# Kernel tuning notes

Measured on AMD Instinct MI355X. Metric: run time of the kernel, lower is better.

The kernel has to match this reference:

```python
import jax, jax.numpy as jnp
import numpy as np

SPARSITY = 0.5  # cur_sparsity set during training; 0.0 default would make masking a no-op
WEIGHT_BETA = 1.0
MASK_ALPHA1 = 1.0
MASK_ALPHA2 = 1.0


def binarize(mask_scores, sparsity):
    # SparseBinarizer.forward: prune (set to 0) the `num_prune` smallest scores globally.
    num_prune = int(mask_scores.size * sparsity)  # static: sparsity is a Python float
    flat = mask_scores.reshape(-1)
    prune_idx = jnp.argsort(flat)[:num_prune]
    mask = jnp.ones_like(flat).at[prune_idx].set(0.0)
    return mask.reshape(mask_scores.shape)


def setup_inputs() -> dict:
    key = jax.random.key(0)
    ks = jax.random.split(key, 9)
    out_f, in_f, r = 4096, 4096, 8
    tokens = 8192  # batch 4 * seq 2048
    return {
        "x": jax.random.normal(ks[0], (tokens, in_f), dtype=jnp.float32),
        "weight": jax.random.normal(ks[1], (out_f, in_f), dtype=jnp.float32) * 0.02,
        "bias": jax.random.normal(ks[2], (out_f,), dtype=jnp.float32) * 0.02,
        "weight_U": jax.random.normal(ks[3], (out_f, r), dtype=jnp.float32),
        "weight_V": jnp.zeros((r, in_f), dtype=jnp.float32),
        "mask_scores_A": jax.random.normal(ks[4], (out_f, r), dtype=jnp.float32),
        "mask_scores_B": jnp.zeros((r, in_f), dtype=jnp.float32),
        "mask_scores_R": jnp.zeros((out_f,), dtype=jnp.float32),
        "mask_scores_C": jnp.zeros((in_f,), dtype=jnp.float32),
    }


def reference(x, weight, bias, weight_U, weight_V, mask_scores_A, mask_scores_B,
              mask_scores_R, mask_scores_C):
    # weight = W + beta * U @ V   (low-rank weight reconstruction)
    w = weight + WEIGHT_BETA * (weight_U @ weight_V)
    # mask_scores = |w| + a1 * A @ B + a2 * (R[:,None] + C[None,:])
    mask_scores = (jnp.abs(w)
                   + MASK_ALPHA1 * (mask_scores_A @ mask_scores_B)
                   + MASK_ALPHA2 * (mask_scores_R[:, None] + mask_scores_C[None, :]))
    mask = binarize(mask_scores, SPARSITY)
    masked_weight = mask * w  # [out_f, in_f]
    # nn.Linear: x @ W^T + b
    return x @ masked_weight.T + bias
```

## Files before the change

### kernel.cpp

```cpp
#include <hip/hip_runtime.h>
#include <stdint.h>

#define TOKENS 8192
#define OUT_F  4096
#define IN_F   4096
#define RNK    8
#define KPRUNE 8388608u
#define CAP3   16384u

typedef unsigned short u16;
typedef float  f32x4  __attribute__((ext_vector_type(4)));
typedef short  bf16x8 __attribute__((ext_vector_type(8)));
typedef unsigned short u16x4 __attribute__((ext_vector_type(4)));
typedef unsigned short u16x8 __attribute__((ext_vector_type(8)));

#define XB_OFF    0ull
#define WB_OFF    67108864ull
#define CTL_OFF   100663296ull
#define H1_OFF    0
#define H2_OFF    16384
#define CNT3_OFF  32768
#define LIST3_OFF 32772
#define CTL_ZERO_U32 8193

__device__ __forceinline__ u16 f2bf(float f) {
    uint32_t u = __float_as_uint(f);
    u += 0x7fffu + ((u >> 16) & 1u);
    return (u16)(u >> 16);
}

__device__ __forceinline__ uint32_t fkey(float s) {
    uint32_t u = __float_as_uint(s);
    return (u & 0x80000000u) ? ~u : (u | 0x80000000u);
}

__device__ __forceinline__ void hsel(const uint32_t* __restrict__ hist, uint32_t k,
                                     volatile uint32_t* scr,
                                     uint32_t& bin, uint32_t& below)
{
    const int t = threadIdx.x;
    const int lane = t & 63, w = t >> 6;
    uint32_t v[16]; uint32_t s = 0;
#pragma unroll
    for (int j = 0; j < 16; ++j) { v[j] = hist[t*16 + j]; s += v[j]; }
    uint32_t sc = s;
#pragma unroll
    for (int d = 1; d < 64; d <<= 1) {
        uint32_t o = __shfl_up(sc, d, 64);
        if (lane >= d) sc += o;
    }
    if (lane == 63) scr[w] = sc;
    __syncthreads();
    uint32_t woff = 0;
    for (int ww = 0; ww < w; ++ww) woff += scr[ww];
    const uint32_t pre = woff + sc - s;
    if (pre < k && pre + s >= k) {
        uint32_t bb = pre;
#pragma unroll
        for (int j = 0; j < 16; ++j) {
            if (bb < k && bb + v[j] >= k) { scr[4] = (uint32_t)(t*16 + j); scr[5] = bb; }
            bb += v[j];
        }
    }
    __syncthreads();
    bin = scr[4]; below = scr[5];
    __syncthreads();
}

struct S2 { float4 w0, w1; uint4 k0, k1; };
__device__ __forceinline__ S2 score2(const float* __restrict__ W,
                                     const float* __restrict__ V,
                                     const float* __restrict__ B,
                                     const float* __restrict__ C,
                                     const float* uu0, const float* uu1,
                                     const float* aa0, const float* aa1,
                                     float ro0, float ro1, int o0, int i)
{
    const float4 cc = *(const float4*)&C[i];
    float4 w0 = *(const float4*)&W[(size_t)o0*IN_F + i];
    float4 w1 = *(const float4*)&W[(size_t)(o0+1)*IN_F + i];
#pragma unroll
    for (int r = 0; r < RNK; ++r) {
        const float4 v4 = *(const float4*)&V[r*IN_F + i];
        const float a0 = uu0[r], a1 = uu1[r];
        w0.x = fmaf(a0, v4.x, w0.x); w0.y = fmaf(a0, v4.y, w0.y);
        w0.z = fmaf(a0, v4.z, w0.z); w0.w = fmaf(a0, v4.w, w0.w);
        w1.x = fmaf(a1, v4.x, w1.x); w1.y = fmaf(a1, v4.y, w1.y);
        w1.z = fmaf(a1, v4.z, w1.z); w1.w = fmaf(a1, v4.w, w1.w);
    }
    float4 s0, s1;
    s0.x = fabsf(w0.x); s0.y = fabsf(w0.y); s0.z = fabsf(w0.z); s0.w = fabsf(w0.w);
    s1.x = fabsf(w1.x); s1.y = fabsf(w1.y); s1.z = fabsf(w1.z); s1.w = fabsf(w1.w);
#pragma unroll
    for (int r = 0; r < RNK; ++r) {
        const float4 b4 = *(const float4*)&B[r*IN_F + i];
        const float a0 = aa0[r], a1 = aa1[r];
        s0.x = fmaf(a0, b4.x, s0.x); s0.y = fmaf(a0, b4.y, s0.y);
        s0.z = fmaf(a0, b4.z, s0.z); s0.w = fmaf(a0, b4.w, s0.w);
        s1.x = fmaf(a1, b4.x, s1.x); s1.y = fmaf(a1, b4.y, s1.y);
        s1.z = fmaf(a1, b4.z, s1.z); s1.w = fmaf(a1, b4.w, s1.w);
    }
    s0.x += ro0 + cc.x; s0.y += ro0 + cc.y; s0.z += ro0 + cc.z; s0.w += ro0 + cc.w;
    s1.x += ro1 + cc.x; s1.y += ro1 + cc.y; s1.z += ro1 + cc.z; s1.w += ro1 + cc.w;
    S2 o;
    o.w0 = w0; o.w1 = w1;
    o.k0.x = fkey(s0.x); o.k0.y = fkey(s0.y); o.k0.z = fkey(s0.z); o.k0.w = fkey(s0.w);
    o.k1.x = fkey(s1.x); o.k1.y = fkey(s1.y); o.k1.z = fkey(s1.z); o.k1.w = fkey(s1.w);
    return o;
}

#define LOAD_ROWPARAMS                                                        \
    float uu0[RNK], uu1[RNK], aa0[RNK], aa1[RNK];                             \
    _Pragma("unroll") for (int r = 0; r < RNK; ++r) {                         \
        uu0[r] = U[o0*RNK + r];   uu1[r] = U[(o0+1)*RNK + r];                 \
        aa0[r] = A[o0*RNK + r];   aa1[r] = A[(o0+1)*RNK + r];                 \
    }                                                                         \
    const float ro0 = R[o0], ro1 = R[o0 + 1];

__global__ void convx_kernel(const float* __restrict__ x, u16* __restrict__ xB,
                             uint32_t* __restrict__ ctl)
{
    const int t = threadIdx.x;
    if (blockIdx.x < 33) {
        const int i = blockIdx.x * 256 + t;
        if (i < CTL_ZERO_U32) ctl[i] = 0u;
    }
    const size_t idx = (size_t)blockIdx.x * 256 + t;
    const float4* xv = (const float4*)x;
    float4 a = xv[idx*2];
    float4 b = xv[idx*2 + 1];
    u16x8 o;
    o[0]=f2bf(a.x); o[1]=f2bf(a.y); o[2]=f2bf(a.z); o[3]=f2bf(a.w);
    o[4]=f2bf(b.x); o[5]=f2bf(b.y); o[6]=f2bf(b.z); o[7]=f2bf(b.w);
    *((u16x8*)xB + idx) = o;
}

__global__ void prep_kernel(const float* __restrict__ W, const float* __restrict__ U,
                            const float* __restrict__ V, const float* __restrict__ A,
                            const float* __restrict__ B, const float* __restrict__ R,
                            const float* __restrict__ C, uint32_t* __restrict__ hist1)
{
    __shared__ uint32_t lh[4096];
    const int o0 = blockIdx.x * 2, t = threadIdx.x;
    for (int b = t; b < 4096; b += 256) lh[b] = 0u;
    LOAD_ROWPARAMS
    __syncthreads();
    for (int j = 0; j < IN_F/1024; ++j) {
        const int i = j*1024 + t*4;
        S2 s = score2(W, V, B, C, uu0, uu1, aa0, aa1, ro0, ro1, o0, i);
        atomicAdd(&lh[s.k0.x >> 20], 1u); atomicAdd(&lh[s.k0.y >> 20], 1u);
        atomicAdd(&lh[s.k0.z >> 20], 1u); atomicAdd(&lh[s.k0.w >> 20], 1u);
        atomicAdd(&lh[s.k1.x >> 20], 1u); atomicAdd(&lh[s.k1.y >> 20], 1u);
        atomicAdd(&lh[s.k1.z >> 20], 1u); atomicAdd(&lh[s.k1.w >> 20], 1u);
    }
    __syncthreads();
    for (int b = t; b < 4096; b += 256) { uint32_t c = lh[b]; if (c) atomicAdd(&hist1[b], c); }
}

__global__ void hist2r_kernel(const float* __restrict__ W, const float* __restrict__ U,
                              const float* __restrict__ V, const float* __restrict__ A,
                              const float* __restrict__ B, const float* __restrict__ R,
                              const float* __restrict__ C, const uint32_t* __restrict__ hist1,
                              uint32_t* __restrict__ hist2)
{
    __shared__ uint32_t lh[4096];
    __shared__ uint32_t scr[6];
    const int o0 = blockIdx.x * 2, t = threadIdx.x;
    uint32_t b1, below1;
    hsel(hist1, KPRUNE, scr, b1, below1);
    for (int b = t; b < 4096; b += 256) lh[b] = 0u;
    LOAD_ROWPARAMS
    __syncthreads();
    for (int j = 0; j < IN_F/1024; ++j) {
        const int i = j*1024 + t*4;
        S2 s = score2(W, V, B, C, uu0, uu1, aa0, aa1, ro0, ro1, o0, i);
        if ((s.k0.x >> 20) == b1) atomicAdd(&lh[(s.k0.x >> 8) & 0xFFFu], 1u);
        if ((s.k0.y >> 20) == b1) atomicAdd(&lh[(s.k0.y >> 8) & 0xFFFu], 1u);
        if ((s.k0.z >> 20) == b1) atomicAdd(&lh[(s.k0.z >> 8) & 0xFFFu], 1u);
        if ((s.k0.w >> 20) == b1) atomicAdd(&lh[(s.k0.w >> 8) & 0xFFFu], 1u);
        if ((s.k1.x >> 20) == b1) atomicAdd(&lh[(s.k1.x >> 8) & 0xFFFu], 1u);
        if ((s.k1.y >> 20) == b1) atomicAdd(&lh[(s.k1.y >> 8) & 0xFFFu], 1u);
        if ((s.k1.z >> 20) == b1) atomicAdd(&lh[(s.k1.z >> 8) & 0xFFFu], 1u);
        if ((s.k1.w >> 20) == b1) atomicAdd(&lh[(s.k1.w >> 8) & 0xFFFu], 1u);
    }
    __syncthreads();
    for (int b = t; b < 4096; b += 256) { uint32_t c = lh[b]; if (c) atomicAdd(&hist2[b], c); }
}

__global__ void applyr_kernel(const float* __restrict__ W, const float* __restrict__ U,
                              const float* __restrict__ V, const float* __restrict__ A,
                              const float* __restrict__ B, const float* __restrict__ R,
                              const float* __restrict__ C, const uint32_t* __restrict__ hist1,
                              const uint32_t* __restrict__ hist2, u16* __restrict__ wB,
                              uint32_t* __restrict__ cnt3, uint32_t* __restrict__ list3)
{
    __shared__ uint32_t scr[6];
    const int o0 = blockIdx.x * 2, t = threadIdx.x;
    uint32_t b1, below1, b2, below2;
    hsel(hist1, KPRUNE, scr, b1, below1);
    hsel(hist2, KPRUNE - below1, scr, b2, below2);
    const uint32_t pfx = (b1 << 12) | b2;
    LOAD_ROWPARAMS
    for (int j = 0; j < IN_F/1024; ++j) {
        const int i = j*1024 + t*4;
        S2 s = score2(W, V, B, C, uu0, uu1, aa0, aa1, ro0, ro1, o0, i);
        const float w0a[4] = {s.w0.x, s.w0.y, s.w0.z, s.w0.w};
        const float w1a[4] = {s.w1.x, s.w1.y, s.w1.z, s.w1.w};
        const uint32_t k0a[4] = {s.k0.x, s.k0.y, s.k0.z, s.k0.w};
        const uint32_t k1a[4] = {s.k1.x, s.k1.y, s.k1.z, s.k1.w};
        u16x4 b0, b1v;
#pragma unroll
        for (int e = 0; e < 4; ++e) {
            const uint32_t hi = k0a[e] >> 8;
            b0[e] = (hi < pfx) ? (u16)0 : f2bf(w0a[e]);
            if (hi == pfx) {
                uint32_t sl = atomicAdd(cnt3, 1u);
                if (sl < CAP3) list3[sl] = ((uint32_t)(o0*IN_F + i + e) << 8) | (k0a[e] & 0xFFu);
            }
        }
#pragma unroll
        for (int e = 0; e < 4; ++e) {
            const uint32_t hi = k1a[e] >> 8;
            b1v[e] = (hi < pfx) ? (u16)0 : f2bf(w1a[e]);
            if (hi == pfx) {
                uint32_t sl = atomicAdd(cnt3, 1u);
                if (sl < CAP3) list3[sl] = ((uint32_t)((o0+1)*IN_F + i + e) << 8) | (k1a[e] & 0xFFu);
            }
        }
        *(u16x4*)&wB[(size_t)o0*IN_F + i]     = b0;
        *(u16x4*)&wB[(size_t)(o0+1)*IN_F + i] = b1v;
    }
}

__global__ void selfix_kernel(const uint32_t* __restrict__ hist1, const uint32_t* __restrict__ hist2,
                              const uint32_t* __restrict__ cnt3, const uint32_t* __restrict__ list3,
                              u16* __restrict__ wB)
{
    __shared__ uint32_t lst[CAP3];
    __shared__ uint32_t lhist[256];
    __shared__ uint32_t sv[2];
    __shared__ uint32_t scr[6];
    const int t = threadIdx.x;
    uint32_t b1, below1, b2, below2;
    hsel(hist1, KPRUNE, scr, b1, below1);
    hsel(hist2, KPRUNE - below1, scr, b2, below2);
    const uint32_t k3 = KPRUNE - below1 - below2;
    uint32_t n = *cnt3; if (n > CAP3) n = CAP3;
    lhist[t] = 0u;
    __syncthreads();
    for (uint32_t i = t; i < n; i += 256) {
        const uint32_t e = list3[i];
        lst[i] = e;
        atomicAdd(&lhist[e & 0xFFu], 1u);
    }
    __syncthreads();
    uint32_t pre = 0;
    for (int b = 0; b < t; ++b) pre += lhist[b];
    if (pre < k3 && pre + lhist[t] >= k3) {
        sv[0] = (uint32_t)t;
        sv[1] = k3 - pre;
    }
    __syncthreads();
    const uint32_t b3 = sv[0], p = sv[1];
    for (uint32_t i = t; i < n; i += 256) {
        const uint32_t e = lst[i];
        const uint32_t lo = e & 0xFFu;
        if (lo < b3) { wB[e >> 8] = 0u; continue; }
        if (lo != b3) continue;
        uint32_t rank = 0;
        for (uint32_t j = 0; j < n; ++j) {
            const uint32_t f = lst[j];
            rank += ((f & 0xFFu) == b3 && f < e) ? 1u : 0u;
        }
        if (rank < p) wB[e >> 8] = 0u;
    }
}

#define A0H0   0
#define A0H1_0 16384
#define A0H1_1 32768
#define B0S    49152
#define A1H0   81920
#define A1H1_0 98304
#define A1H1_1 114688
#define B1S    131072

__device__ __forceinline__ void gl_lds16(const char* src, char* dst) {
    __builtin_amdgcn_global_load_lds((const __attribute__((address_space(1))) void*)src,
                                     (__attribute__((address_space(3))) void*)dst, 16, 0, 0);
}

__global__ __launch_bounds__(512, 2) void gemm256_kernel(const u16* __restrict__ xB,
                                                         const u16* __restrict__ wB,
                                                         const float* __restrict__ bias,
                                                         float* __restrict__ out)
{
    __shared__ char ldsc[163840];
    const int t    = threadIdx.x;
    const int lane = t & 63;
    const int wid  = t >> 6;
    const int wm   = wid >> 2;
    const int wn   = wid & 3;
    const int bid  = blockIdx.x;
    const int bn   = bid & 15;
    const int bm   = bid >> 4;

    const int l15 = lane & 15;
    const int kb  = (lane >> 4) << 4;
    const int rowA = 16*wm + l15;
    const int rowB = (wn & 1)*64 + l15;
    const int baseA = rowA*64 + (kb ^ (((rowA >> 1) & 3) << 4));
    const int baseB = rowB*64 + (kb ^ (((rowB >> 1) & 3) << 4));
    const char* aB0 = ldsc + baseA;
    const char* aB1 = ldsc + A1H0 + baseA;
    const char* bB0 = ldsc + B0S + (wn >> 1)*16384 + baseB;
    const char* bB1 = bB0 + (B1S - B0S);

    const int scol = ((t & 3) * 16) ^ (((t >> 3) & 3) << 4);
    const char* pA = (const char*)xB + ((size_t)(bm*256 + (t >> 2))) * (IN_F*2) + scol;
    const char* pB = (const char*)wB + ((size_t)(bn*256 + (t >> 2))) * (IN_F*2) + scol;
    const int tb16 = t * 16;

#define STAGEH(pG, slot, h, tile) do {                                        \
    const char* _s = (pG) + (size_t)(tile)*128 + (size_t)(h)*(128*IN_F*2);    \
    char* _d = ldsc + (slot) + tb16;                                          \
    gl_lds16(_s, _d);                                                         \
    gl_lds16(_s + 64, _d + 8192);                                             \
} while (0)

    f32x4  acc[8][4] = {};
    bf16x8 b[4][2];
    bf16x8 a[2][2];

#define LOADB(bp) do {                                                        \
    _Pragma("unroll") for (int ni = 0; ni < 4; ++ni)                          \
    _Pragma("unroll") for (int kk = 0; kk < 2; ++kk)                          \
        b[ni][kk] = *(const bf16x8*)((bp) + ni*1024 + kk*8192);               \
} while (0)

#define LOADA(ap, slot, q, mo) do {                                           \
    _Pragma("unroll") for (int mm = 0; mm < 2; ++mm)                          \
    _Pragma("unroll") for (int kk = 0; kk < 2; ++kk)                          \
        a[mm][kk] = *(const bf16x8*)((ap) + (slot) +                          \
                      (2*(q)+mm-(mo))*2048 + kk*8192);                        \
} while (0)

#define MFMAQ(q) do {                                                         \
    _Pragma("unroll") for (int mm = 0; mm < 2; ++mm)                          \
    _Pragma("unroll") for (int ni = 0; ni < 4; ++ni)                          \
    _Pragma("unroll") for (int kk = 0; kk < 2; ++kk)                          \
        acc[2*(q)+mm][ni] = __builtin_amdgcn_mfma_f32_16x16x32_bf16(          \
            a[mm][kk], b[ni][kk], acc[2*(q)+mm][ni], 0, 0, 0);                \
} while (0)

#define PH_TAIL(q)                                                            \
    __builtin_amdgcn_s_barrier();                                             \
    asm volatile("s_waitcnt lgkmcnt(0)" ::: "memory");                        \
    __builtin_amdgcn_s_setprio(1);                                            \
    MFMAQ(q);                                                                 \
    __builtin_amdgcn_s_setprio(0);                                            \
    __builtin_amdgcn_s_barrier();

#define STQ(q) do {                                                           \
    _Pragma("unroll") for (int mm = 0; mm < 2; ++mm) {                        \
        const int r0 = orow0 + 32*(2*(q)+mm);                                 \
        _Pragma("unroll") for (int ni = 0; ni < 4; ++ni) {                    \
            f32x4 v = acc[2*(q)+mm][ni];                                      \
            const int col = ocol0 + ni*16;                                    \
            _Pragma("unroll") for (int e = 0; e < 4; ++e)                     \
                out[(size_t)(r0 + e)*OUT_F + col] = v[e] + bv[ni];            \
        }                                                                     \
    }                                                                         \
} while (0)

#define PH_TAIL_ST(q)                                                         \
    __builtin_amdgcn_s_barrier();                                             \
    asm volatile("s_waitcnt lgkmcnt(0)" ::: "memory");                        \
    __builtin_amdgcn_s_setprio(1);                                            \
    MFMAQ(q);                                                                 \
    __builtin_amdgcn_s_setprio(0);                                            \
    STQ(q);                                                                   \
    __builtin_amdgcn_s_barrier();

    STAGEH(pA, A0H1_0, 1, 0);
    STAGEH(pB, B0S,         0, 0);
    STAGEH(pB, B0S + 16384, 1, 0);
    STAGEH(pA, A0H0, 0, 0);
    STAGEH(pA, A1H1_0, 1, 1);
    STAGEH(pB, B1S,         0, 1);
    STAGEH(pB, B1S + 16384, 1, 1);
    STAGEH(pA, A1H0, 0, 1);
    asm volatile("s_waitcnt vmcnt(8)" ::: "memory");
    __builtin_amdgcn_s_barrier();

#pragma unroll 1
    for (int j = 0; j < 31; ++j) {
        const int se = 2*j + 2;
        const int so = 2*j + 3;
        const int pc = j & 1;
        const int a0h1c = pc ? A0H1_1 : A0H1_0;
        const int a0h1n = pc ? A0H1_0 : A0H1_1;
        const int a1h1c = pc ? A1H1_1 : A1H1_0;
        const int a1h1n = pc ? A1H1_0 : A1H1_1;

        LOADB(bB0); LOADA(aB0, A0H0, 0, 0);
        STAGEH(pA, a0h1n, 1, se);
        asm volatile("s_waitcnt lgkmcnt(8)" ::: "memory");
        PH_TAIL(0)
        LOADA(aB0, A0H0, 1, 0);
        STAGEH(pB, B0S, 0, se);
        PH_TAIL(1)
        LOADA(aB0, a0h1c, 2, 4);
        STAGEH(pB, B0S + 16384, 1, se);
        PH_TAIL(2)
        LOADA(aB0, a0h1c, 3, 4);
        STAGEH(pA, A0H0, 0, se);
        asm volatile("s_waitcnt vmcnt(8)" ::: "memory");
        PH_TAIL(3)

        LOADB(bB1); LOADA(aB1, 0, 0, 0);
        STAGEH(pA, a1h1n, 1, so);
        asm volatile("s_waitcnt lgkmcnt(8)" ::: "memory");
        PH_TAIL(0)
        LOADA(aB1, 0, 1, 0);
        STAGEH(pB, B1S, 0, so);
        PH_TAIL(1)
        LOADA(aB1, a1h1c - A1H0, 2, 4);
        STAGEH(pB, B1S + 16384, 1, so);
        PH_TAIL(2)
        LOADA(aB1, a1h1c - A1H0, 3, 4);
        STAGEH(pA, A1H0, 0, so);
        asm volatile("s_waitcnt vmcnt(8)" ::: "memory");
        PH_TAIL(3)
    }

    const int orow0 = bm*256 + 16*wm + ((lane >> 4) << 2);
    const int ocol0 = bn*256 + 64*wn + l15;
    float bv[4];
#pragma unroll
    for (int ni = 0; ni < 4; ++ni) bv[ni] = bias[ocol0 + ni*16];

    LOADB(bB0); LOADA(aB0, A0H0, 0, 0);
    asm volatile("s_waitcnt lgkmcnt(8)" ::: "memory");
    PH_TAIL(0)
    LOADA(aB0, A0H0, 1, 0);
    PH_TAIL(1)
    LOADA(aB0, A0H1_1, 2, 4);
    PH_TAIL(2)
    LOADA(aB0, A0H1_1, 3, 4);
    PH_TAIL(3)

    asm volatile("s_waitcnt vmcnt(0)" ::: "memory");
    __builtin_amdgcn_s_barrier();
    LOADB(bB1); LOADA(aB1, 0, 0, 0);
    asm volatile("s_waitcnt lgkmcnt(8)" ::: "memory");
    PH_TAIL_ST(0)
    LOADA(aB1, 0, 1, 0);
    PH_TAIL_ST(1)
    LOADA(aB1, A1H1_1 - A1H0, 2, 4);
    PH_TAIL_ST(2)
    LOADA(aB1, A1H1_1 - A1H0, 3, 4);
    PH_TAIL_ST(3)

#undef STAGEH
#undef LOADB
#undef LOADA
#undef MFMAQ
#undef PH_TAIL
#undef PH_TAIL_ST
#undef STQ
}

extern "C" void kernel_launch(void* const* d_in, const int* in_sizes, int n_in,
                              void* d_out, int out_size, void* d_ws, size_t ws_size,
                              hipStream_t stream)
{
    const float* x    = (const float*)d_in[0];
    const float* W    = (const float*)d_in[1];
    const float* bias = (const float*)d_in[2];
    const float* U    = (const float*)d_in[3];
    const float* V    = (const float*)d_in[4];
    const float* A    = (const float*)d_in[5];
    const float* B    = (const float*)d_in[6];
    const float* R    = (const float*)d_in[7];
    const float* C    = (const float*)d_in[8];
    float* out = (float*)d_out;

    char* ws = (char*)d_ws;
    u16*      xB    = (u16*)(ws + XB_OFF);
    u16*      wB    = (u16*)(ws + WB_OFF);
    uint32_t* ctl   = (uint32_t*)(ws + CTL_OFF);
    uint32_t* h1    = (uint32_t*)((char*)ctl + H1_OFF);
    uint32_t* h2    = (uint32_t*)((char*)ctl + H2_OFF);
    uint32_t* cnt3  = (uint32_t*)((char*)ctl + CNT3_OFF);
    uint32_t* list3 = (uint32_t*)((char*)ctl + LIST3_OFF);

    convx_kernel<<<TOKENS*IN_F/8/256, 256, 0, stream>>>(x, xB, ctl);
    prep_kernel<<<OUT_F/2, 256, 0, stream>>>(W, U, V, A, B, R, C, h1);
    hist2r_kernel<<<OUT_F/2, 256, 0, stream>>>(W, U, V, A, B, R, C, h1, h2);
    applyr_kernel<<<OUT_F/2, 256, 0, stream>>>(W, U, V, A, B, R, C, h1, h2, wB, cnt3, list3);
    selfix_kernel<<<1, 256, 0, stream>>>(h1, h2, cnt3, list3, wB);
    gemm256_kernel<<<(TOKENS/256)*(OUT_F/256), 512, 0, stream>>>(xB, wB, bias, out);
}
```

Baseline: 382.5 us.

## Interleave x bf16 conversion blocks into the mask-score passes

The standalone x-to-bf16 conversion kernel is split into chunks spread across the prep, hist2 and apply kernels. Extra blocks in each of those launches convert slices of x, with block indices interleaved among the score blocks, and a tiny kernel now zeroes the control area. The aim is to overlap the memory-bound conversion with the compute and atomic-heavy score passes and drop a full launch. The cost is more complex block-index mapping and conversion blocks contending with the score blocks for bandwidth and CU slots.

```diff
diff --git a/kernel.cpp b/kernel.cpp
--- a/kernel.cpp
+++ b/kernel.cpp
@@ -117,15 +117,10 @@
     }                                                                         \
     const float ro0 = R[o0], ro1 = R[o0 + 1];
 
-__global__ void convx_kernel(const float* __restrict__ x, u16* __restrict__ xB,
-                             uint32_t* __restrict__ ctl)
-{
-    const int t = threadIdx.x;
-    if (blockIdx.x < 33) {
-        const int i = blockIdx.x * 256 + t;
-        if (i < CTL_ZERO_U32) ctl[i] = 0u;
-    }
-    const size_t idx = (size_t)blockIdx.x * 256 + t;
+__device__ __forceinline__ void convx_chunk(const float* __restrict__ x,
+                                            u16* __restrict__ xB, int cid)
+{
+    const size_t idx = (size_t)cid * 256 + threadIdx.x;
     const float4* xv = (const float4*)x;
     float4 a = xv[idx*2];
     float4 b = xv[idx*2 + 1];
@@ -135,13 +130,22 @@
     *((u16x8*)xB + idx) = o;
 }
 
+__global__ void zero_kernel(uint32_t* __restrict__ ctl)
+{
+    const int i = blockIdx.x * 256 + threadIdx.x;
+    if (i < CTL_ZERO_U32) ctl[i] = 0u;
+}
+
 __global__ void prep_kernel(const float* __restrict__ W, const float* __restrict__ U,
                             const float* __restrict__ V, const float* __restrict__ A,
                             const float* __restrict__ B, const float* __restrict__ R,
-                            const float* __restrict__ C, uint32_t* __restrict__ hist1)
+                            const float* __restrict__ C, const float* __restrict__ x,
+                            u16* __restrict__ xB, uint32_t* __restrict__ hist1)
 {
     __shared__ uint32_t lh[4096];
-    const int o0 = blockIdx.x * 2, t = threadIdx.x;
+    const int bid = blockIdx.x;
+    if (bid & 3) { convx_chunk(x, xB, bid - (bid >> 2) - 1); return; }
+    const int o0 = (bid >> 2) * 2, t = threadIdx.x;
     for (int b = t; b < 4096; b += 256) lh[b] = 0u;
     LOAD_ROWPARAMS
     __syncthreads();
@@ -160,12 +164,15 @@
 __global__ void hist2r_kernel(const float* __restrict__ W, const float* __restrict__ U,
                               const float* __restrict__ V, const float* __restrict__ A,
                               const float* __restrict__ B, const float* __restrict__ R,
-                              const float* __restrict__ C, const uint32_t* __restrict__ hist1,
+                              const float* __restrict__ C, const float* __restrict__ x,
+                              u16* __restrict__ xB, const uint32_t* __restrict__ hist1,
                               uint32_t* __restrict__ hist2)
 {
     __shared__ uint32_t lh[4096];
     __shared__ uint32_t scr[6];
-    const int o0 = blockIdx.x * 2, t = threadIdx.x;
+    const int bid = blockIdx.x;
+    if (bid & 3) { convx_chunk(x, xB, 6144 + bid - (bid >> 2) - 1); return; }
+    const int o0 = (bid >> 2) * 2, t = threadIdx.x;
     uint32_t b1, below1;
     hsel(hist1, KPRUNE, scr, b1, below1);
     for (int b = t; b < 4096; b += 256) lh[b] = 0u;
@@ -190,12 +197,15 @@
 __global__ void applyr_kernel(const float* __restrict__ W, const float* __restrict__ U,
                               const float* __restrict__ V, const float* __restrict__ A,
                               const float* __restrict__ B, const float* __restrict__ R,
-                              const float* __restrict__ C, const uint32_t* __restrict__ hist1,
+                              const float* __restrict__ C, const float* __restrict__ x,
+                              u16* __restrict__ xB, const uint32_t* __restrict__ hist1,
                               const uint32_t* __restrict__ hist2, u16* __restrict__ wB,
                               uint32_t* __restrict__ cnt3, uint32_t* __restrict__ list3)
 {
     __shared__ uint32_t scr[6];
-    const int o0 = blockIdx.x * 2, t = threadIdx.x;
+    const int bid = blockIdx.x;
+    if (bid % 3) { convx_chunk(x, xB, 12288 + bid - bid/3 - 1); return; }
+    const int o0 = (bid / 3) * 2, t = threadIdx.x;
     uint32_t b1, below1, b2, below2;
     hsel(hist1, KPRUNE, scr, b1, below1);
     hsel(hist2, KPRUNE - below1, scr, b2, below2);
@@ -495,10 +505,10 @@
     uint32_t* cnt3  = (uint32_t*)((char*)ctl + CNT3_OFF);
     uint32_t* list3 = (uint32_t*)((char*)ctl + LIST3_OFF);
 
-    convx_kernel<<<TOKENS*IN_F/8/256, 256, 0, stream>>>(x, xB, ctl);
-    prep_kernel<<<OUT_F/2, 256, 0, stream>>>(W, U, V, A, B, R, C, h1);
-    hist2r_kernel<<<OUT_F/2, 256, 0, stream>>>(W, U, V, A, B, R, C, h1, h2);
-    applyr_kernel<<<OUT_F/2, 256, 0, stream>>>(W, U, V, A, B, R, C, h1, h2, wB, cnt3, list3);
+    zero_kernel<<<33, 256, 0, stream>>>(ctl);
+    prep_kernel<<<8192, 256, 0, stream>>>(W, U, V, A, B, R, C, x, xB, h1);
+    hist2r_kernel<<<8192, 256, 0, stream>>>(W, U, V, A, B, R, C, x, xB, h1, h2);
+    applyr_kernel<<<6144, 256, 0, stream>>>(W, U, V, A, B, R, C, x, xB, h1, h2, wB, cnt3, list3);
     selfix_kernel<<<1, 256, 0, stream>>>(h1, h2, cnt3, list3, wB);
     gemm256_kernel<<<(TOKENS/256)*(OUT_F/256), 512, 0, stream>>>(xB, wB, bias, out);
 }
```

After: 501.4 us. +31.1%, slower.
